# Optimization experiments

Measured on AMD Instinct MI355X. Metric: run time of the kernel, lower is better.

The kernel has to match this reference:

```python
import jax, jax.numpy as jnp
import numpy as np

NUM_OUT_EDGES = 2
NUM_INTERMEDIATE = 2
NUM_FSM_STATES = NUM_OUT_EDGES + NUM_INTERMEDIATE  # S = 4
NUM_EDGE_TYPES = 3
NUM_VARIANTS = 4
NUM_NODE_TYPES = 8
NUM_NODES = 256
BACKTRACK_FAILS_PROB = 0.001
EDGE_PROB = 0.05  # avg degree ~ 12.8 per edge type


def setup_inputs() -> dict:
    key = jax.random.key(0)
    k1, k2, k3, k4 = jax.random.split(key, 4)
    vw = jax.random.uniform(k1, (NUM_NODES, NUM_NODES, NUM_VARIANTS))
    vw = vw / jnp.sum(vw, axis=-1, keepdims=True)  # nonneg, sums to 1 on last axis
    adjacency = (jax.random.uniform(k2, (NUM_EDGE_TYPES, NUM_NODES, NUM_NODES)) < EDGE_PROB).astype(jnp.float32)
    n_actions = NUM_EDGE_TYPES * NUM_FSM_STATES + 3  # moves + ACCEPT/BACKTRACK/FAIL
    log_routing_params = 0.5 * jax.random.normal(
        k3, (NUM_VARIANTS, NUM_NODE_TYPES, NUM_FSM_STATES, n_actions))
    node_types = jax.random.randint(k4, (NUM_NODES,), 0, NUM_NODE_TYPES)
    return {
        'variant_weights': vw,
        'adjacency': adjacency,
        'log_routing_params': log_routing_params,
        'node_types': node_types,
        'steps': 48,
    }


def _forward(variant_weights, adjacency, log_routing_params, node_types, steps):
    N = variant_weights.shape[0]
    S, T, E = NUM_FSM_STATES, NUM_EDGE_TYPES, NUM_OUT_EDGES
    dt = variant_weights.dtype

    # Row-normalized per-edge-type adjacency (uniform over typed successors;
    deg = jnp.sum(adjacency, axis=-1, keepdims=True)
    a_norm = adjacency / jnp.maximum(deg, 1.0)  # [T, N, N]

    # routing_softmax over actions; policy conditioned on (variant, node type, fsm state)
    policy = jax.nn.softmax(log_routing_params, axis=-1)  # [V, NT, S, A]
    pol_n = policy[:, node_types]                          # [V, N, S, A]

    # Mix policy variants per (start node i, current node j)
    mixed = jnp.einsum('ijv,vjsa->ijsa', variant_weights, pol_n)  # [N, N, S, A]
    p_move = mixed[..., :T * S].reshape(N, N, S, T, S)  # MOVE(edge type t, next state u)
    p_accept = mixed[..., T * S]                        # ACCEPT at current node
    p_back = mixed[..., T * S + 1]                      # BACKTRACK to start node

    # Start states: edge type e starts in fsm state e at node i (one-hot).
    eyeS = jnp.eye(S, dtype=dt)[:E]  # [E, S]
    eyeN = jnp.eye(N, dtype=dt)      # [N, N]
    dist0 = eyeS[:, None, :, None] * eyeN[None, :, None, :]  # [E, N, S, N]
    restart = dist0 * (1.0 - BACKTRACK_FAILS_PROB)

    def step(carry, _):
        dist, accept = carry  # dist: [E, N_start, S, N_cur], accept: [E, N, N]
        accept = accept + jnp.einsum('eisj,ijs->eij', dist, p_accept)
        back = jnp.einsum('eisj,ijs->ei', dist, p_back)
        tmp = jnp.einsum('eisj,ijstu->eituj', dist, p_move)   # pick edge type + next state
        moved = jnp.einsum('eituj,tjk->eiuk', tmp, a_norm)    # move along typed edges
        dist = moved + back[:, :, None, None] * restart
        return (dist, accept), None

    accept0 = jnp.zeros((E, N, N), dt)
    (dist, accept), _ = jax.lax.scan(step, (dist0, accept0), None, length=steps)
    # absorb remaining accept probability after final transition
    accept = accept + jnp.einsum('eisj,ijs->eij', dist, p_accept)
    return accept  # [num_out_edges, num_nodes, num_nodes]


def reference(variant_weights, adjacency, log_routing_params, node_types, steps):
    return _forward(variant_weights, adjacency, log_routing_params, node_types, steps)
```

## Files before the change

kernel.cpp:

```cpp
#include <hip/hip_runtime.h>
#include <hip/hip_fp16.h>

#define NN    256
#define SS    4
#define TT    3
#define VV    4
#define NTY   8
#define NAC   15
#define CAPG  48
#define CAPE  (CAPG * 2)
#define ROWB  40
#define ZROWB (NN * ROWB)
#define BUFB  (ZROWB + ROWB)
#define ZPK   ((unsigned)ZROWB | ((unsigned)ZROWB << 16))
#define GMAXR 32

typedef _Float16 h2v __attribute__((ext_vector_type(2)));

#if defined(__has_builtin)
#if __has_builtin(__builtin_amdgcn_fdot2)
#define HAVE_FDOT2 1
#endif
#endif

static __device__ __forceinline__ unsigned ph2(float a, float b) {
    union { __half2 h; unsigned u; } c;
    c.h = __floats2half2_rn(a, b);
    return c.u;
}
static __device__ __forceinline__ h2v bch2(unsigned u) {
    union { unsigned u; h2v h; } c; c.u = u; return c.h;
}
static __device__ __forceinline__ float2 h2f2(unsigned u) {
    union { unsigned u; __half2 h; } c; c.u = u; return __half22float2(c.h);
}

__global__ void k_setup(const float* __restrict__ adj,
                        const float* __restrict__ lrp,
                        float* __restrict__ inv_deg,
                        float* __restrict__ pol,
                        unsigned* __restrict__ epk,
                        int* __restrict__ gcnt) {
    const int b = blockIdx.x;
    const int tid = threadIdx.x;

    if (b < TT * NN) {
        __shared__ float wsum[4];
        float s = adj[(size_t)b * NN + tid];
#pragma unroll
        for (int off = 32; off > 0; off >>= 1) s += __shfl_down(s, off, 64);
        if ((tid & 63) == 0) wsum[tid >> 6] = s;
        __syncthreads();
        if (tid == 0)
            inv_deg[b] = 1.0f / fmaxf(wsum[0] + wsum[1] + wsum[2] + wsum[3], 1.0f);
    } else if (b < TT * NN + NN) {
        __shared__ int cnt;
        __shared__ unsigned short offs[CAPE + 2];
        const int col = b - TT * NN;
        if (tid == 0) cnt = 0;
        __syncthreads();
#pragma unroll
        for (int t = 0; t < TT; t++) {
            float a = adj[((size_t)t * NN + tid) * NN + col];
            if (a != 0.f) {
                int idx = atomicAdd(&cnt, 1);
                if (idx < CAPE) offs[idx] = (unsigned short)(tid * ROWB + t * 8);
            }
        }
        __syncthreads();
        int c = cnt; if (c > CAPE) c = CAPE;
        if (tid == 0 && (c & 1)) offs[c] = (unsigned short)ZROWB;
        __syncthreads();
        const int g = (c + 1) >> 1;
        for (int gg = tid; gg < g; gg += blockDim.x)
            epk[(size_t)gg * NN + col] =
                (unsigned)offs[2 * gg] | ((unsigned)offs[2 * gg + 1] << 16);
        if (tid == 0) gcnt[col] = g;
    } else {
        if (tid < VV * NTY * SS) {
            float x[NAC]; float m = -3.4e38f;
#pragma unroll
            for (int a = 0; a < NAC; a++) { x[a] = lrp[tid * NAC + a]; m = fmaxf(m, x[a]); }
            float ssum = 0.f;
#pragma unroll
            for (int a = 0; a < NAC; a++) { x[a] = __expf(x[a] - m); ssum += x[a]; }
            float inv = 1.f / ssum;
#pragma unroll
            for (int a = 0; a < NAC; a++) pol[tid * NAC + a] = x[a] * inv;
        }
    }
}

__global__ __launch_bounds__(256, 2) void k_main(
    const float* __restrict__ vw,
    const int* __restrict__ node_types,
    const float* __restrict__ pol,
    const float* __restrict__ inv_deg,
    const unsigned* __restrict__ epk,
    const int* __restrict__ gcnt,
    const int* __restrict__ steps_p,
    float* __restrict__ out)
{
    const int i    = blockIdx.x & 255;
    const int e    = blockIdx.x >> 8;
    const int col  = threadIdx.x;
    const int wv   = col >> 6;
    const int lane = col & 63;
    const int steps = steps_p[0];

    __shared__ __align__(16) char tmpb[2 * BUFB];
    __shared__ float backp[2][4];

    if (col < 20) {
        int pb = col / 10, w = col % 10;
        ((unsigned*)(tmpb + pb * BUFB + ZROWB))[w] = 0u;
    }

    const float4 w4 = *(const float4*)(vw + ((size_t)i * NN + col) * VV);
    const float wvv[VV] = {w4.x, w4.y, w4.z, w4.w};
    const int ntj = node_types[col];
    float pmS[SS][12], pacc[SS], pback[SS];
#pragma unroll
    for (int s = 0; s < SS; s++) {
        pacc[s] = 0.f; pback[s] = 0.f;
#pragma unroll
        for (int a = 0; a < 12; a++) pmS[s][a] = 0.f;
    }
#pragma unroll
    for (int v = 0; v < VV; v++) {
        const float* pr = pol + (size_t)(v * NTY + ntj) * SS * NAC;
#pragma unroll
        for (int s = 0; s < SS; s++) {
            const float* p = pr + s * NAC;
#pragma unroll
            for (int a = 0; a < 12; a++) pmS[s][a] = fmaf(wvv[v], p[a], pmS[s][a]);
            pacc[s]  = fmaf(wvv[v], p[12], pacc[s]);
            pback[s] = fmaf(wvv[v], p[13], pback[s]);
        }
    }
    {
        float invd[TT];
#pragma unroll
        for (int t = 0; t < TT; t++) invd[t] = inv_deg[t * NN + col];
#pragma unroll
        for (int s = 0; s < SS; s++)
#pragma unroll
            for (int a = 0; a < 12; a++) pmS[s][a] *= invd[a >> 2];
    }

    float D0 = (0 == e && col == i) ? 1.f : 0.f;
    float D1 = (1 == e && col == i) ? 1.f : 0.f;
    float D2 = 0.f, D3 = 0.f;
    float acc = 0.f;

    const int g_all = gcnt[col];
    int gm = g_all;
#pragma unroll
    for (int off = 32; off > 0; off >>= 1) {
        int o = __shfl_xor(gm, off, 64);
        gm = o > gm ? o : gm;
    }
    const int gmax = __builtin_amdgcn_readfirstlane(gm);

    unsigned ep[GMAXR];
#pragma unroll
    for (int g = 0; g < GMAXR; g++) {
        unsigned pk = epk[(size_t)g * NN + col];
        ep[g] = (g < g_all) ? pk : ZPK;
    }

    const h2v S10 = {(_Float16)1.0f, (_Float16)0.0f};
    const h2v S01 = {(_Float16)0.0f, (_Float16)1.0f};
    char* const myrow0 = tmpb + col * ROWB;

    for (int step = 0; step < steps; step++) {
        const int par = step & 1;
        char* const buf = tmpb + par * BUFB;

        float ad = D0 * pacc[0];
        ad = fmaf(D1, pacc[1], ad); ad = fmaf(D2, pacc[2], ad); ad = fmaf(D3, pacc[3], ad);
        acc += ad;
        float bj = D0 * pback[0];
        bj = fmaf(D1, pback[1], bj); bj = fmaf(D2, pback[2], bj); bj = fmaf(D3, pback[3], bj);

        float tv[12];
#pragma unroll
        for (int a = 0; a < 12; a++) {
            float x = D0 * pmS[0][a];
            x = fmaf(D1, pmS[1][a], x);
            x = fmaf(D2, pmS[2][a], x);
            x = fmaf(D3, pmS[3][a], x);
            tv[a] = x;
        }
        char* const myrow = myrow0 + par * BUFB;
        uint2 wA; wA.x = ph2(tv[0], tv[1]);  wA.y = ph2(tv[2],  tv[3]);
        uint2 wB; wB.x = ph2(tv[4], tv[5]);  wB.y = ph2(tv[6],  tv[7]);
        uint2 wC; wC.x = ph2(tv[8], tv[9]);  wC.y = ph2(tv[10], tv[11]);
        *(uint2*)(myrow)      = wA;
        *(uint2*)(myrow + 8)  = wB;
        *(uint2*)(myrow + 16) = wC;

#pragma unroll
        for (int off = 32; off > 0; off >>= 1) bj += __shfl_down(bj, off, 64);
        if (lane == 0) backp[par][wv] = bj;

        __syncthreads();

        float d0a = 0.f, d1a = 0.f, d2a = 0.f, d3a = 0.f;
        float d0b = 0.f, d1b = 0.f, d2b = 0.f, d3b = 0.f;
#pragma unroll
        for (int g = 0; g < GMAXR; g++) {
            if (g < gmax) {
                const unsigned pk = ep[g];
                const uint2 q0 = *(const uint2*)(buf + (pk & 0xffffu));
                const uint2 q1 = *(const uint2*)(buf + (pk >> 16));
#ifdef HAVE_FDOT2
                if (g & 1) {
                    d0b = __builtin_amdgcn_fdot2(bch2(q0.x), S10, d0b, false);
                    d1b = __builtin_amdgcn_fdot2(bch2(q0.x), S01, d1b, false);
                    d2b = __builtin_amdgcn_fdot2(bch2(q0.y), S10, d2b, false);
                    d3b = __builtin_amdgcn_fdot2(bch2(q0.y), S01, d3b, false);
                    d0b = __builtin_amdgcn_fdot2(bch2(q1.x), S10, d0b, false);
                    d1b = __builtin_amdgcn_fdot2(bch2(q1.x), S01, d1b, false);
                    d2b = __builtin_amdgcn_fdot2(bch2(q1.y), S10, d2b, false);
                    d3b = __builtin_amdgcn_fdot2(bch2(q1.y), S01, d3b, false);
                } else {
                    d0a = __builtin_amdgcn_fdot2(bch2(q0.x), S10, d0a, false);
                    d1a = __builtin_amdgcn_fdot2(bch2(q0.x), S01, d1a, false);
                    d2a = __builtin_amdgcn_fdot2(bch2(q0.y), S10, d2a, false);
                    d3a = __builtin_amdgcn_fdot2(bch2(q0.y), S01, d3a, false);
                    d0a = __builtin_amdgcn_fdot2(bch2(q1.x), S10, d0a, false);
                    d1a = __builtin_amdgcn_fdot2(bch2(q1.x), S01, d1a, false);
                    d2a = __builtin_amdgcn_fdot2(bch2(q1.y), S10, d2a, false);
                    d3a = __builtin_amdgcn_fdot2(bch2(q1.y), S01, d3a, false);
                }
#else
                float2 f0 = h2f2(q0.x), f1 = h2f2(q0.y), f2 = h2f2(q1.x), f3 = h2f2(q1.y);
                if (g & 1) {
                    d0b += f0.x + f2.x; d1b += f0.y + f2.y;
                    d2b += f1.x + f3.x; d3b += f1.y + f3.y;
                } else {
                    d0a += f0.x + f2.x; d1a += f0.y + f2.y;
                    d2a += f1.x + f3.x; d3a += f1.y + f3.y;
                }
#endif
            }
        }
        for (int g = GMAXR; g < gmax; g++) {
            unsigned pk = epk[(size_t)g * NN + col];
            pk = (g < g_all) ? pk : ZPK;
            const uint2 q0 = *(const uint2*)(buf + (pk & 0xffffu));
            const uint2 q1 = *(const uint2*)(buf + (pk >> 16));
            float2 f0 = h2f2(q0.x), f1 = h2f2(q0.y), f2 = h2f2(q1.x), f3 = h2f2(q1.y);
            d0a += f0.x + f2.x; d1a += f0.y + f2.y;
            d2a += f1.x + f3.x; d3a += f1.y + f3.y;
        }

        float d0 = d0a + d0b, d1 = d1a + d1b, d2 = d2a + d2b, d3 = d3a + d3b;

        if (col == i) {
            const float* bp = backp[par];
            float back = bp[0] + bp[1] + bp[2] + bp[3];
            if (e == 0) d0 = fmaf(back, 0.999f, d0);
            else        d1 = fmaf(back, 0.999f, d1);
        }
        D0 = d0; D1 = d1; D2 = d2; D3 = d3;
    }

    float ad = D0 * pacc[0];
    ad = fmaf(D1, pacc[1], ad); ad = fmaf(D2, pacc[2], ad); ad = fmaf(D3, pacc[3], ad);
    acc += ad;
    out[((size_t)e * NN + i) * NN + col] = acc;
}

extern "C" void kernel_launch(void* const* d_in, const int* in_sizes, int n_in,
                              void* d_out, int out_size, void* d_ws, size_t ws_size,
                              hipStream_t stream) {
    const float* vw  = (const float*)d_in[0];
    const float* adj = (const float*)d_in[1];
    const float* lrp = (const float*)d_in[2];
    const int* node_types = (const int*)d_in[3];
    const int* steps_p    = (const int*)d_in[4];

    float* ws       = (float*)d_ws;
    float* pol      = ws;
    float* inv_deg  = ws + 1920;
    int*   gcnt     = (int*)(ws + 2688);
    unsigned* epk   = (unsigned*)(ws + 2944);

    k_setup<<<TT * NN + NN + 1, 256, 0, stream>>>(adj, lrp, inv_deg, pol, epk, gcnt);
    k_main<<<2 * NN, 256, 0, stream>>>(vw, node_types, pol, inv_deg, epk, gcnt,
                                       steps_p, (float*)d_out);
}
```

Measured before the change: 184.3 us.

## Sort columns by edge-group count per block, pad LDS rows, unroll parity

Each block builds a counting-sort permutation of its columns by gcnt (edge-group count, descending), so the threads in a wavefront have similar gather loop trip counts and waste less time on divergence. The LDS row stride grows from 40 to 44 bytes to reduce bank conflicts on the gathered reads. The step loop is unrolled by two with the buffer parity known at compile time, which removes the runtime parity address math. In exchange there is a short prologue with shared atomics and extra barriers, a slightly larger LDS footprint, and scattered vw/output accesses because each thread's column is now permuted.

After: 572.0 us. 210% more time.

```diff
diff --git a/kernel.cpp b/kernel.cpp
--- a/kernel.cpp
+++ b/kernel.cpp
@@ -1,5 +1,6 @@
 #include <hip/hip_runtime.h>
 #include <hip/hip_fp16.h>
+#include <utility>
 
 #define NN    256
 #define SS    4
@@ -9,7 +10,7 @@
 #define NAC   15
 #define CAPG  48
 #define CAPE  (CAPG * 2)
-#define ROWB  40
+#define ROWB  44
 #define ZROWB (NN * ROWB)
 #define BUFB  (ZROWB + ROWB)
 #define ZPK   ((unsigned)ZROWB | ((unsigned)ZROWB << 16))
@@ -103,16 +104,35 @@
 {
     const int i    = blockIdx.x & 255;
     const int e    = blockIdx.x >> 8;
-    const int col  = threadIdx.x;
-    const int wv   = col >> 6;
-    const int lane = col & 63;
+    const int tid  = threadIdx.x;
+    const int wv   = tid >> 6;
+    const int lane = tid & 63;
     const int steps = steps_p[0];
 
     __shared__ __align__(16) char tmpb[2 * BUFB];
     __shared__ float backp[2][4];
-
-    if (col < 20) {
-        int pb = col / 10, w = col % 10;
+    __shared__ int sperm[NN];
+    __shared__ int shist[CAPG + 2];
+
+    const int myg = gcnt[tid];
+    if (tid < CAPG + 2) shist[tid] = 0;
+    __syncthreads();
+    atomicAdd(&shist[myg], 1);
+    __syncthreads();
+    if (tid == 0) {
+        int accum = 0;
+        for (int g = CAPG + 1; g >= 0; g--) { int c = shist[g]; shist[g] = accum; accum += c; }
+    }
+    __syncthreads();
+    {
+        int pos = atomicAdd(&shist[myg], 1);
+        sperm[pos] = tid;
+    }
+    __syncthreads();
+    const int col = sperm[tid];
+
+    if (tid < 22) {
+        int pb = tid / 11, w = tid % 11;
         ((unsigned*)(tmpb + pb * BUFB + ZROWB))[w] = 0u;
     }
 
@@ -173,9 +193,9 @@
     const h2v S01 = {(_Float16)0.0f, (_Float16)1.0f};
     char* const myrow0 = tmpb + col * ROWB;
 
-    for (int step = 0; step < steps; step++) {
-        const int par = step & 1;
-        char* const buf = tmpb + par * BUFB;
+    auto do_step = [&](auto par_c) {
+        constexpr int PAR = decltype(par_c)::value;
+        char* const buf = tmpb + PAR * BUFB;
 
         float ad = D0 * pacc[0];
         ad = fmaf(D1, pacc[1], ad); ad = fmaf(D2, pacc[2], ad); ad = fmaf(D3, pacc[3], ad);
@@ -192,7 +212,7 @@
             x = fmaf(D3, pmS[3][a], x);
             tv[a] = x;
         }
-        char* const myrow = myrow0 + par * BUFB;
+        char* const myrow = myrow0 + PAR * BUFB;
         uint2 wA; wA.x = ph2(tv[0], tv[1]);  wA.y = ph2(tv[2],  tv[3]);
         uint2 wB; wB.x = ph2(tv[4], tv[5]);  wB.y = ph2(tv[6],  tv[7]);
         uint2 wC; wC.x = ph2(tv[8], tv[9]);  wC.y = ph2(tv[10], tv[11]);
@@ -202,7 +222,7 @@
 
 #pragma unroll
         for (int off = 32; off > 0; off >>= 1) bj += __shfl_down(bj, off, 64);
-        if (lane == 0) backp[par][wv] = bj;
+        if (lane == 0) backp[PAR][wv] = bj;
 
         __syncthreads();
 
@@ -259,13 +279,20 @@
         float d0 = d0a + d0b, d1 = d1a + d1b, d2 = d2a + d2b, d3 = d3a + d3b;
 
         if (col == i) {
-            const float* bp = backp[par];
+            const float* bp = backp[PAR];
             float back = bp[0] + bp[1] + bp[2] + bp[3];
             if (e == 0) d0 = fmaf(back, 0.999f, d0);
             else        d1 = fmaf(back, 0.999f, d1);
         }
         D0 = d0; D1 = d1; D2 = d2; D3 = d3;
-    }
+    };
+
+    int sp = 0;
+    for (; sp + 1 < steps; sp += 2) {
+        do_step(std::integral_constant<int, 0>{});
+        do_step(std::integral_constant<int, 1>{});
+    }
+    if (sp < steps) do_step(std::integral_constant<int, 0>{});
 
     float ad = D0 * pacc[0];
     ad = fmaf(D1, pacc[1], ad); ad = fmaf(D2, pacc[2], ad); ad = fmaf(D3, pacc[3], ad);
```
